# Optimization experiments

Hardware: AMD Instinct MI355X
Metric: run time of the kernel (lower is better)

Reference implementation:

```python
import jax, jax.numpy as jnp
import numpy as np

B, NS, NQ = 128, 128, 512
D_IN, D_OUT = 256, 64


def setup_inputs() -> dict:
    key = jax.random.key(0)
    ks = jax.random.split(key, 6)
    return {
        "phi_support": jax.random.normal(ks[0], (B, NS, D_IN), dtype=jnp.float32),
        "y_support": jax.random.normal(ks[1], (B, NS, D_OUT), dtype=jnp.float32),
        "phi_query": jax.random.normal(ks[2], (B, NQ, D_IN), dtype=jnp.float32),
        "y_query": jax.random.normal(ks[3], (B, NQ, D_OUT), dtype=jnp.float32),
        # xavier-uniform-ish params
        "m_prior": jax.random.uniform(ks[4], (D_IN, D_OUT), minval=-1.0, maxval=1.0) * np.sqrt(6.0 / (D_IN + D_OUT)),
        "S_inv_prior_asym": jax.random.uniform(ks[5], (D_IN, D_IN), minval=-1.0, maxval=1.0) * np.sqrt(6.0 / (2 * D_IN)),
        "sig_eps": jnp.array([0.1], dtype=jnp.float32),
    }


def reference(phi_support, y_support, phi_query, y_query, m_prior, S_inv_prior_asym, sig_eps):
    alpha = 1.0
    d_out = m_prior.shape[1]
    # prior precision (symmetric PSD by construction) and natural-param prior mean
    S_inv_prior = alpha * (S_inv_prior_asym @ S_inv_prior_asym.T)          # [D_in, D_in]
    m_prior_nat = S_inv_prior @ m_prior                                     # [D_in, D_out]
    # posterior precision / covariance per task (nobs > 0 branch)
    S_inv = jnp.einsum('bni,bnj->bij', phi_support, phi_support) + S_inv_prior  # [B, D_in, D_in]
    S = jnp.linalg.inv(S_inv)                                               # batched small inverse
    rhs = jnp.einsum('bni,bnk->bik', phi_support, y_support) + m_prior_nat  # [B, D_in, D_out]
    m = S @ rhs                                                             # [B, D_in, D_out]
    # predictive mean and spread
    mu = phi_query @ m                                                      # [B, Q, D_out]
    spread_fac = 1.0 + jnp.einsum('bqi,bij,bqj->bq', phi_query, S, phi_query)  # [B, Q]
    # sig = spread_fac (x) (eye * sig_eps) : diagonal [B, Q, D_out, D_out]
    diag = jnp.eye(d_out, dtype=mu.dtype) * sig_eps                         # [D_out, D_out]
    sig = spread_fac[..., None, None] * diag
    # nll: logdet of diagonal sig + quadratic form with its inverse (diag -> reciprocal)
    logdet = d_out * (jnp.log(spread_fac) + jnp.log(sig_eps))               # [B, Q]
    resid = y_query - mu
    quadf = jnp.sum(resid * resid, axis=-1) / (spread_fac * sig_eps)        # [B, Q]
    nll = logdet.mean() + quadf.mean()
    return mu, sig, nll
```

## Files before the change

### kernel.cpp

```cpp
#include <hip/hip_runtime.h>
#include <math.h>

#define B_T   128
#define NS    128
#define NQ    512
#define DIN   256
#define DOUT  64

#define MU_SIZE  (B_T*NQ*DOUT)
#define SIG_SIZE (B_T*NQ*DOUT*DOUT)
#define NLL_IDX  (MU_SIZE + SIG_SIZE)

__global__ __launch_bounds__(256) void k_prior_sp(const float* __restrict__ A,
                                                  double* __restrict__ Sp,
                                                  double* __restrict__ NLLACC) {
    __shared__ float Ai[16][260];
    __shared__ float Aj[16][260];
    int bi = blockIdx.x;
    int i0 = (bi >> 4) << 4;
    int j0 = (bi & 15) << 4;
    int tid = threadIdx.x;
    if (bi == 0 && tid == 0) NLLACC[0] = 0.0;
    for (int idx = tid; idx < 16 * 256; idx += 256) {
        int r = idx >> 8, c = idx & 255;
        Ai[r][c] = A[(i0 + r) * 256 + c];
        Aj[r][c] = A[(j0 + r) * 256 + c];
    }
    __syncthreads();
    int r = tid >> 4, c = tid & 15;
    double acc = 0.0;
    for (int k = 0; k < 256; ++k)
        acc += (double)Ai[r][k] * (double)Aj[c][k];
    Sp[(i0 + r) * 256 + (j0 + c)] = acc;
}

__global__ __launch_bounds__(64) void k_prior_mpn(const double* __restrict__ Sp,
                                                  const float* __restrict__ MP,
                                                  double* __restrict__ MPN) {
    int i = blockIdx.x, k = threadIdx.x;
    double acc = 0.0;
    for (int t = 0; t < 256; ++t)
        acc += Sp[i * 256 + t] * (double)MP[t * 64 + k];
    MPN[i * 64 + k] = acc;
}

__global__ __launch_bounds__(256) void k_build_G(const float* __restrict__ PHI,
                                                 const double* __restrict__ Sp,
                                                 double* __restrict__ G) {
    __shared__ float As[128][64];
    __shared__ float Bs[128][64];
    int b = blockIdx.x;
    int by = blockIdx.y;
    int ti = 0;
    while (((ti + 1) * (ti + 2)) / 2 <= by) ti++;
    int tj = by - (ti * (ti + 1)) / 2;
    int i0 = ti * 64, j0 = tj * 64;
    int tid = threadIdx.x;
    const float* Pb = PHI + b * (NS * DIN);
    for (int idx = tid; idx < 128 * 64; idx += 256) {
        int n = idx >> 6, c = idx & 63;
        As[n][c] = Pb[n * 256 + i0 + c];
        Bs[n][c] = Pb[n * 256 + j0 + c];
    }
    __syncthreads();
    int tx = tid & 15, ty = tid >> 4;
    double acc[4][4];
#pragma unroll
    for (int r = 0; r < 4; ++r)
#pragma unroll
        for (int s = 0; s < 4; ++s) acc[r][s] = 0.0;
    for (int n = 0; n < 128; ++n) {
        float a0 = As[n][4 * ty + 0], a1 = As[n][4 * ty + 1];
        float a2 = As[n][4 * ty + 2], a3 = As[n][4 * ty + 3];
        float b0 = Bs[n][4 * tx + 0], b1 = Bs[n][4 * tx + 1];
        float b2 = Bs[n][4 * tx + 2], b3 = Bs[n][4 * tx + 3];
        acc[0][0] += (double)a0 * b0; acc[0][1] += (double)a0 * b1;
        acc[0][2] += (double)a0 * b2; acc[0][3] += (double)a0 * b3;
        acc[1][0] += (double)a1 * b0; acc[1][1] += (double)a1 * b1;
        acc[1][2] += (double)a1 * b2; acc[1][3] += (double)a1 * b3;
        acc[2][0] += (double)a2 * b0; acc[2][1] += (double)a2 * b1;
        acc[2][2] += (double)a2 * b2; acc[2][3] += (double)a2 * b3;
        acc[3][0] += (double)a3 * b0; acc[3][1] += (double)a3 * b1;
        acc[3][2] += (double)a3 * b2; acc[3][3] += (double)a3 * b3;
    }
    double* Gb = G + b * 65536;
#pragma unroll
    for (int r = 0; r < 4; ++r) {
        int i = i0 + 4 * ty + r;
#pragma unroll
        for (int s = 0; s < 4; ++s) {
            int j = j0 + 4 * tx + s;
            Gb[i * 256 + j] = acc[r][s] + Sp[i * 256 + j];
        }
    }
}

__global__ __launch_bounds__(256) void k_build_rhs(const float* __restrict__ PHI,
                                                   const float* __restrict__ Y,
                                                   const double* __restrict__ MPN,
                                                   double* __restrict__ RHS) {
    __shared__ float As[128][64];
    __shared__ float Ys[128][64];
    int b = blockIdx.x, i0 = blockIdx.y * 64, tid = threadIdx.x;
    const float* Pb = PHI + b * (NS * DIN);
    const float* Yb = Y + b * (NS * DOUT);
    for (int idx = tid; idx < 128 * 64; idx += 256) {
        int n = idx >> 6, c = idx & 63;
        As[n][c] = Pb[n * 256 + i0 + c];
        Ys[n][c] = Yb[n * 64 + c];
    }
    __syncthreads();
    int tx = tid & 15, ty = tid >> 4;
    double acc[4][4];
#pragma unroll
    for (int r = 0; r < 4; ++r)
#pragma unroll
        for (int s = 0; s < 4; ++s) acc[r][s] = 0.0;
    for (int n = 0; n < 128; ++n) {
        float a0 = As[n][4 * ty + 0], a1 = As[n][4 * ty + 1];
        float a2 = As[n][4 * ty + 2], a3 = As[n][4 * ty + 3];
        float y0 = Ys[n][4 * tx + 0], y1 = Ys[n][4 * tx + 1];
        float y2 = Ys[n][4 * tx + 2], y3 = Ys[n][4 * tx + 3];
        acc[0][0] += (double)a0 * y0; acc[0][1] += (double)a0 * y1;
        acc[0][2] += (double)a0 * y2; acc[0][3] += (double)a0 * y3;
        acc[1][0] += (double)a1 * y0; acc[1][1] += (double)a1 * y1;
        acc[1][2] += (double)a1 * y2; acc[1][3] += (double)a1 * y3;
        acc[2][0] += (double)a2 * y0; acc[2][1] += (double)a2 * y1;
        acc[2][2] += (double)a2 * y2; acc[2][3] += (double)a2 * y3;
        acc[3][0] += (double)a3 * y0; acc[3][1] += (double)a3 * y1;
        acc[3][2] += (double)a3 * y2; acc[3][3] += (double)a3 * y3;
    }
    double* Rb = RHS + b * 16384;
#pragma unroll
    for (int r = 0; r < 4; ++r) {
        int i = i0 + 4 * ty + r;
#pragma unroll
        for (int s = 0; s < 4; ++s) {
            int kc = 4 * tx + s;
            Rb[i * 64 + kc] = acc[r][s] + MPN[i * 64 + kc];
        }
    }
}

__global__ __launch_bounds__(256) void k_cholinv(double* __restrict__ G,
                                                 double* __restrict__ LT,
                                                 double* __restrict__ TI,
                                                 float* __restrict__ TIF) {
    __shared__ double S[8192];
    int b = blockIdx.x, tid = threadIdx.x;
    double* Gb = G + b * 65536;
    double* LTb = LT + b * 65536;
    double* TIb = TI + b * 65536;
    float* TIFb = TIF + b * 65536;

    double* P = S;
#define PCH(p, r) P[(p) * 258 + (r)]
    for (int k0 = 0; k0 < 256; k0 += 16) {
        int rows = 256 - k0;
        for (int idx = tid; idx < rows * 16; idx += 256) {
            int r = k0 + (idx >> 4), p = idx & 15;
            PCH(p, r) = Gb[r * 256 + k0 + p];
        }
        __syncthreads();
        for (int p = 0; p < 16; ++p) {
            int k = k0 + p;
            if (tid >= k) {
                double v = PCH(p, tid);
                for (int p2 = 0; p2 < p; ++p2) v -= PCH(p2, tid) * PCH(p2, k);
                PCH(p, tid) = v;
            }
            __syncthreads();
            double d = sqrt(fmax(PCH(p, k), 1e-300));
            double inv = 1.0 / d;
            if (tid > k) PCH(p, tid) *= inv;
            else if (tid == k) PCH(p, tid) = d;
            __syncthreads();
        }
        for (int p = 0; p < 16; ++p) {
            int k = k0 + p;
            if (tid >= k) LTb[k * 256 + tid] = PCH(p, tid);
        }
        int ty = tid >> 4, tx = tid & 15;
        for (int i2 = k0 + 16 + 2 * ty; i2 < 256; i2 += 32) {
            double pa[16], pb[16];
#pragma unroll
            for (int p = 0; p < 16; ++p) { pa[p] = PCH(p, i2); pb[p] = PCH(p, i2 + 1); }
            for (int j2 = k0 + 16 + 2 * tx; j2 <= i2 + 1; j2 += 32) {
                double g00 = 0.0, g01 = 0.0, g10 = 0.0, g11 = 0.0;
#pragma unroll
                for (int p = 0; p < 16; ++p) {
                    double q0 = PCH(p, j2), q1 = PCH(p, j2 + 1);
                    g00 += pa[p] * q0; g01 += pa[p] * q1;
                    g10 += pb[p] * q0; g11 += pb[p] * q1;
                }
                if (j2 <= i2)     Gb[i2 * 256 + j2]           -= g00;
                if (j2 + 1 <= i2) Gb[i2 * 256 + j2 + 1]       -= g01;
                Gb[(i2 + 1) * 256 + j2] -= g10;
                if (j2 <= i2)     Gb[(i2 + 1) * 256 + j2 + 1] -= g11;
            }
        }
        __syncthreads();
    }
#undef PCH

    double* SHD = S;
    for (int idx = tid; idx < 65536; idx += 256) {
        int i = idx >> 8, k = idx & 255;
        if (k > i) { TIb[idx] = 0.0; TIFb[idx] = 0.0f; }
    }
    for (int idx = tid; idx < 8192; idx += 256) {
        int g = idx >> 10, rem = idx & 1023, k = rem >> 5, i = rem & 31;
        SHD[idx] = LTb[(32 * g + k) * 256 + 32 * g + i];
    }
    __syncthreads();
    {
        int g = tid >> 5, j = tid & 31;
        const double* D = SHD + g * 1024;
        double x[32];
#pragma unroll
        for (int i = 0; i < 32; ++i) {
            double s = (i == j) ? 1.0 : 0.0;
#pragma unroll
            for (int k = 0; k < i; ++k) {
                double lv = D[k * 32 + i];
                s -= (k >= j) ? lv * x[k] : 0.0;
            }
            double inv = 1.0 / D[i * 32 + i];
            x[i] = (i >= j) ? s * inv : 0.0;
        }
#pragma unroll
        for (int i = 0; i < 32; ++i) {
            int gi = 32 * g + i, gj = 32 * g + j;
            TIb[gi * 256 + gj] = x[i];
            TIFb[gi * 256 + gj] = (float)x[i];
        }
    }
    __syncthreads();
    double* Bsh = SHD;
    int j = tid & 31, ig = tid >> 5;
    for (int I = 1; I < 8; ++I) {
        for (int J = I - 1; J >= 0; --J) {
            double acc[4] = {0.0, 0.0, 0.0, 0.0};
            for (int K = J; K < I; ++K) {
                for (int kk = 0; kk < 32; ++kk) {
                    double tv = TIb[(32 * K + kk) * 256 + 32 * J + j];
#pragma unroll
                    for (int r = 0; r < 4; ++r) {
                        double lv = LTb[(32 * K + kk) * 256 + 32 * I + ig * 4 + r];
                        acc[r] += lv * tv;
                    }
                }
            }
            __syncthreads();
#pragma unroll
            for (int r = 0; r < 4; ++r) Bsh[(ig * 4 + r) * 32 + j] = acc[r];
            __syncthreads();
            double c[4] = {0.0, 0.0, 0.0, 0.0};
            for (int k = 0; k < 32; ++k) {
                double bv = Bsh[k * 32 + j];
#pragma unroll
                for (int r = 0; r < 4; ++r) {
                    double dv = TIb[(32 * I + ig * 4 + r) * 256 + 32 * I + k];
                    c[r] -= dv * bv;
                }
            }
#pragma unroll
            for (int r = 0; r < 4; ++r) {
                int gi = 32 * I + ig * 4 + r, gj = 32 * J + j;
                TIb[gi * 256 + gj] = c[r];
                TIFb[gi * 256 + gj] = (float)c[r];
            }
        }
        __syncthreads();
    }
}

__global__ __launch_bounds__(256) void k_gemm_Z(const double* __restrict__ TI,
                                                const double* __restrict__ RHS,
                                                double* __restrict__ Z) {
    __shared__ double As[32][64];
    __shared__ double Bs[64][64];
    int b = blockIdx.x, i0 = blockIdx.y * 32;
    int tid = threadIdx.x, c = tid & 63, rg = tid >> 6;
    const double* TIb = TI + b * 65536;
    const double* Rb = RHS + b * 16384;
    double* Zb = Z + b * 16384;
    double acc[8] = {};
    for (int k0 = 0; k0 <= i0; k0 += 64) {
        for (int idx = tid; idx < 2048; idx += 256) {
            int r = idx >> 6, kk = idx & 63;
            As[r][kk] = TIb[(i0 + r) * 256 + k0 + kk];
        }
        for (int idx = tid; idx < 4096; idx += 256) {
            int kk = idx >> 6, cc = idx & 63;
            Bs[kk][cc] = Rb[(k0 + kk) * 64 + cc];
        }
        __syncthreads();
        for (int kk = 0; kk < 64; ++kk) {
            double bv = Bs[kk][c];
#pragma unroll
            for (int r = 0; r < 8; ++r)
                acc[r] += As[rg * 8 + r][kk] * bv;
        }
        __syncthreads();
    }
#pragma unroll
    for (int r = 0; r < 8; ++r)
        Zb[(i0 + rg * 8 + r) * 64 + c] = acc[r];
}

__global__ __launch_bounds__(256) void k_gemm_M(const double* __restrict__ TI,
                                                const double* __restrict__ Z,
                                                double* __restrict__ M) {
    __shared__ double As[64][32];
    __shared__ double Bs[64][64];
    int b = blockIdx.x, i0 = blockIdx.y * 32;
    int tid = threadIdx.x, c = tid & 63, rg = tid >> 6;
    const double* TIb = TI + b * 65536;
    const double* Zb = Z + b * 16384;
    double* Mb = M + b * 16384;
    double acc[8] = {};
    for (int k0 = (i0 >> 6) << 6; k0 < 256; k0 += 64) {
        for (int idx = tid; idx < 2048; idx += 256) {
            int kk = idx >> 5, ri = idx & 31;
            As[kk][ri] = TIb[(k0 + kk) * 256 + i0 + ri];
        }
        for (int idx = tid; idx < 4096; idx += 256) {
            int kk = idx >> 6, cc = idx & 63;
            Bs[kk][cc] = Zb[(k0 + kk) * 64 + cc];
        }
        __syncthreads();
        for (int kk = 0; kk < 64; ++kk) {
            double bv = Bs[kk][c];
#pragma unroll
            for (int r = 0; r < 8; ++r)
                acc[r] += As[kk][rg * 8 + r] * bv;
        }
        __syncthreads();
    }
#pragma unroll
    for (int r = 0; r < 8; ++r)
        Mb[(i0 + rg * 8 + r) * 64 + c] = acc[r];
}

__global__ __launch_bounds__(256) void k_spread_gemm(const float* __restrict__ PHIQ,
                                                     const float* __restrict__ TIF,
                                                     float* __restrict__ PSUM) {
    __shared__ float Qs[64][65];
    __shared__ float Ts[64][65];
    int b = blockIdx.x, q0 = blockIdx.y * 64, I = blockIdx.z, i0 = I * 64;
    int tid = threadIdx.x, tx = tid & 15, ty = tid >> 4;
    const float* Qb = PHIQ + b * (NQ * DIN) + q0 * DIN;
    const float* Tb = TIF + b * 65536;
    float acc[4][4];
#pragma unroll
    for (int r = 0; r < 4; ++r)
#pragma unroll
        for (int s = 0; s < 4; ++s) acc[r][s] = 0.0f;
    for (int k0 = 0; k0 <= i0; k0 += 64) {
        for (int idx = tid; idx < 4096; idx += 256) {
            int r = idx >> 6, c = idx & 63;
            Qs[r][c] = Qb[r * 256 + k0 + c];
            Ts[c][r] = Tb[(i0 + r) * 256 + k0 + c];
        }
        __syncthreads();
        for (int kk = 0; kk < 64; ++kk) {
            float a0 = Qs[4 * ty + 0][kk], a1 = Qs[4 * ty + 1][kk];
            float a2 = Qs[4 * ty + 2][kk], a3 = Qs[4 * ty + 3][kk];
            float b0 = Ts[kk][4 * tx + 0], b1 = Ts[kk][4 * tx + 1];
            float b2 = Ts[kk][4 * tx + 2], b3 = Ts[kk][4 * tx + 3];
            acc[0][0] += a0 * b0; acc[0][1] += a0 * b1; acc[0][2] += a0 * b2; acc[0][3] += a0 * b3;
            acc[1][0] += a1 * b0; acc[1][1] += a1 * b1; acc[1][2] += a1 * b2; acc[1][3] += a1 * b3;
            acc[2][0] += a2 * b0; acc[2][1] += a2 * b1; acc[2][2] += a2 * b2; acc[2][3] += a2 * b3;
            acc[3][0] += a3 * b0; acc[3][1] += a3 * b1; acc[3][2] += a3 * b2; acc[3][3] += a3 * b3;
        }
        __syncthreads();
    }
#pragma unroll
    for (int r = 0; r < 4; ++r) {
        float p = acc[r][0] * acc[r][0] + acc[r][1] * acc[r][1]
                + acc[r][2] * acc[r][2] + acc[r][3] * acc[r][3];
        p += __shfl_down(p, 8, 16);
        p += __shfl_down(p, 4, 16);
        p += __shfl_down(p, 2, 16);
        p += __shfl_down(p, 1, 16);
        if (tx == 0) PSUM[(size_t)(b * 4 + I) * 512 + q0 + 4 * ty + r] = p;
    }
}

__global__ __launch_bounds__(256) void k_mu_nll(const float* __restrict__ PHIQ,
                                                const double* __restrict__ M,
                                                const float* __restrict__ YQ,
                                                const float* __restrict__ PSUM,
                                                const float* __restrict__ SE,
                                                float* __restrict__ SPREAD,
                                                double* __restrict__ NLLACC,
                                                float* __restrict__ MU) {
    __shared__ float Qs[64][65];
    __shared__ float Ms[64][64];
    __shared__ double nred[64];
    int b = blockIdx.x, q0 = blockIdx.y * 64, tid = threadIdx.x;
    int tx = tid & 15, ty = tid >> 4;
    const float* Qb = PHIQ + b * (NQ * DIN) + q0 * DIN;
    const double* Mb = M + b * 16384;
    float acc[4][4];
#pragma unroll
    for (int r = 0; r < 4; ++r)
#pragma unroll
        for (int s = 0; s < 4; ++s) acc[r][s] = 0.0f;
    for (int c0 = 0; c0 < 256; c0 += 64) {
        for (int idx = tid; idx < 4096; idx += 256) {
            int r = idx >> 6, c = idx & 63;
            Qs[r][c] = Qb[r * 256 + c0 + c];
            Ms[r][c] = (float)Mb[(c0 + r) * 64 + c];
        }
        __syncthreads();
        for (int kk = 0; kk < 64; ++kk) {
            float a0 = Qs[4 * ty + 0][kk], a1 = Qs[4 * ty + 1][kk];
            float a2 = Qs[4 * ty + 2][kk], a3 = Qs[4 * ty + 3][kk];
            float b0 = Ms[kk][4 * tx + 0], b1 = Ms[kk][4 * tx + 1];
            float b2 = Ms[kk][4 * tx + 2], b3 = Ms[kk][4 * tx + 3];
            acc[0][0] += a0 * b0; acc[0][1] += a0 * b1; acc[0][2] += a0 * b2; acc[0][3] += a0 * b3;
            acc[1][0] += a1 * b0; acc[1][1] += a1 * b1; acc[1][2] += a1 * b2; acc[1][3] += a1 * b3;
            acc[2][0] += a2 * b0; acc[2][1] += a2 * b1; acc[2][2] += a2 * b2; acc[2][3] += a2 * b3;
            acc[3][0] += a3 * b0; acc[3][1] += a3 * b1; acc[3][2] += a3 * b2; acc[3][3] += a3 * b3;
        }
        __syncthreads();
    }
    float se = SE[0];
#pragma unroll
    for (int r = 0; r < 4; ++r) {
        int q = q0 + 4 * ty + r;
        float4 v = make_float4(acc[r][0], acc[r][1], acc[r][2], acc[r][3]);
        *(float4*)&MU[(b * NQ + q) * 64 + 4 * tx] = v;
        float4 y = *(const float4*)&YQ[(size_t)(b * NQ + q) * 64 + 4 * tx];
        float dx = y.x - v.x, dy = y.y - v.y, dz = y.z - v.z, dw = y.w - v.w;
        float qs = dx * dx + dy * dy + dz * dz + dw * dw;
        qs += __shfl_down(qs, 8, 16);
        qs += __shfl_down(qs, 4, 16);
        qs += __shfl_down(qs, 2, 16);
        qs += __shfl_down(qs, 1, 16);
        if (tx == 0) {
            float sp = 1.0f + PSUM[(size_t)(b * 4 + 0) * 512 + q]
                            + PSUM[(size_t)(b * 4 + 1) * 512 + q]
                            + PSUM[(size_t)(b * 4 + 2) * 512 + q]
                            + PSUM[(size_t)(b * 4 + 3) * 512 + q];
            SPREAD[b * 512 + q] = sp;
            float val = 64.0f * (logf(sp) + logf(se)) + qs / (sp * se);
            nred[ty * 4 + r] = (double)val;
        }
    }
    __syncthreads();
    for (int s = 32; s > 0; s >>= 1) {
        if (tid < s) nred[tid] += nred[tid + s];
        __syncthreads();
    }
    if (tid == 0) atomicAdd(NLLACC, nred[0] * (1.0 / 65536.0));
}

__global__ void k_nll_final(const double* __restrict__ NLLACC,
                            float* __restrict__ out) {
    if (threadIdx.x == 0) out[NLL_IDX] = (float)NLLACC[0];
}

__global__ __launch_bounds__(256) void k_sig(const float* __restrict__ SPREAD,
                                             const float* __restrict__ SE,
                                             float* __restrict__ out) {
    __shared__ float sv_s;
    int bq = blockIdx.x, tid = threadIdx.x;
    if (tid == 0) sv_s = SPREAD[bq] * SE[0];
    __syncthreads();
    float sv = sv_s;
    float* base = out + (size_t)MU_SIZE + (size_t)bq * 4096;
    int i = tid >> 2;
    int jb = (tid & 3) << 4;
    int d = i - jb;
    float vals[16];
#pragma unroll
    for (int t = 0; t < 16; ++t) vals[t] = (t == d) ? sv : 0.0f;
    float4* p = (float4*)(base + tid * 16);
    p[0] = make_float4(vals[0], vals[1], vals[2], vals[3]);
    p[1] = make_float4(vals[4], vals[5], vals[6], vals[7]);
    p[2] = make_float4(vals[8], vals[9], vals[10], vals[11]);
    p[3] = make_float4(vals[12], vals[13], vals[14], vals[15]);
}

extern "C" void kernel_launch(void* const* d_in, const int* in_sizes, int n_in,
                              void* d_out, int out_size, void* d_ws, size_t ws_size,
                              hipStream_t stream) {
    const float* PHI_S = (const float*)d_in[0];
    const float* Y_S   = (const float*)d_in[1];
    const float* PHI_Q = (const float*)d_in[2];
    const float* Y_Q   = (const float*)d_in[3];
    const float* MP    = (const float*)d_in[4];
    const float* AP    = (const float*)d_in[5];
    const float* SE    = (const float*)d_in[6];
    float* out = (float*)d_out;

    double* scratch = (double*)(out + MU_SIZE);
    double* G    = scratch;
    double* LT   = G + 8388608;
    double* RHS  = LT + 8388608;
    double* Z    = RHS + 2097152;
    double* TI   = Z + 2097152;
    double* Spd  = TI + 8388608;
    double* MPN  = Spd + 65536;
    float*  TIF  = (float*)(MPN + 16384);
    float*  PSUM = TIF + 8388608;
    float*  SPREAD = (float*)d_ws;
    double* NLLACC = (double*)((char*)d_ws + 65536 * 4);

    k_prior_sp   <<<256, 256, 0, stream>>>(AP, Spd, NLLACC);
    k_prior_mpn  <<<256, 64, 0, stream>>>(Spd, MP, MPN);
    k_build_G    <<<dim3(B_T, 10), 256, 0, stream>>>(PHI_S, Spd, G);
    k_build_rhs  <<<dim3(B_T, 4), 256, 0, stream>>>(PHI_S, Y_S, MPN, RHS);
    k_cholinv    <<<B_T, 256, 0, stream>>>(G, LT, TI, TIF);
    k_gemm_Z     <<<dim3(B_T, 8), 256, 0, stream>>>(TI, RHS, Z);
    k_gemm_M     <<<dim3(B_T, 8), 256, 0, stream>>>(TI, Z, RHS);
    k_spread_gemm<<<dim3(B_T, 8, 4), 256, 0, stream>>>(PHI_Q, TIF, PSUM);
    k_mu_nll     <<<dim3(B_T, 8), 256, 0, stream>>>(PHI_Q, RHS, Y_Q, PSUM, SE,
                                                    SPREAD, NLLACC, out);
    k_nll_final  <<<1, 64, 0, stream>>>(NLLACC, out);
    k_sig        <<<65536, 256, 0, stream>>>(SPREAD, SE, out);
}
```

Measured before the change: 2.244 ms.

## Widen Cholesky panel to 32 columns and fold small prior kernels into neighbors

The blocked Cholesky panel width grows from 16 to 32, which halves the number of panel iterations and global trailing-update passes over G, at the cost of more per-thread registers (32-element pa/pb arrays) and more serial per-column work in the panel. The prior mean-natural-param GEMM moves into extra blocks of k_build_rhs, and its addition is deferred to k_gemm_Z's load. The nll final write moves into k_sig, which removes two tiny launches. Index arithmetic in mu output also switches to size_t.

```diff
diff --git a/kernel.cpp b/kernel.cpp
--- a/kernel.cpp
+++ b/kernel.cpp
@@ -32,16 +32,6 @@
     for (int k = 0; k < 256; ++k)
         acc += (double)Ai[r][k] * (double)Aj[c][k];
     Sp[(i0 + r) * 256 + (j0 + c)] = acc;
-}
-
-__global__ __launch_bounds__(64) void k_prior_mpn(const double* __restrict__ Sp,
-                                                  const float* __restrict__ MP,
-                                                  double* __restrict__ MPN) {
-    int i = blockIdx.x, k = threadIdx.x;
-    double acc = 0.0;
-    for (int t = 0; t < 256; ++t)
-        acc += Sp[i * 256 + t] * (double)MP[t * 64 + k];
-    MPN[i * 64 + k] = acc;
 }
 
 __global__ __launch_bounds__(256) void k_build_G(const float* __restrict__ PHI,
@@ -97,11 +87,25 @@
 
 __global__ __launch_bounds__(256) void k_build_rhs(const float* __restrict__ PHI,
                                                    const float* __restrict__ Y,
-                                                   const double* __restrict__ MPN,
-                                                   double* __restrict__ RHS) {
+                                                   const float* __restrict__ MP,
+                                                   const double* __restrict__ Sp,
+                                                   double* __restrict__ RHS,
+                                                   double* __restrict__ MPNo) {
+    int b = blockIdx.x, by = blockIdx.y, tid = threadIdx.x;
+    if (by == 4) {
+        if (b >= 4) return;
+        for (int out = tid; out < 4096; out += 256) {
+            int r = 64 * b + (out >> 6), cc = out & 63;
+            double acc = 0.0;
+            for (int t = 0; t < 256; ++t)
+                acc += Sp[r * 256 + t] * (double)MP[t * 64 + cc];
+            MPNo[r * 64 + cc] = acc;
+        }
+        return;
+    }
     __shared__ float As[128][64];
     __shared__ float Ys[128][64];
-    int b = blockIdx.x, i0 = blockIdx.y * 64, tid = threadIdx.x;
+    int i0 = by * 64;
     const float* Pb = PHI + b * (NS * DIN);
     const float* Yb = Y + b * (NS * DOUT);
     for (int idx = tid; idx < 128 * 64; idx += 256) {
@@ -135,10 +139,8 @@
     for (int r = 0; r < 4; ++r) {
         int i = i0 + 4 * ty + r;
 #pragma unroll
-        for (int s = 0; s < 4; ++s) {
-            int kc = 4 * tx + s;
-            Rb[i * 64 + kc] = acc[r][s] + MPN[i * 64 + kc];
-        }
+        for (int s = 0; s < 4; ++s)
+            Rb[i * 64 + 4 * tx + s] = acc[r][s];
     }
 }
 
@@ -146,7 +148,7 @@
                                                  double* __restrict__ LT,
                                                  double* __restrict__ TI,
                                                  float* __restrict__ TIF) {
-    __shared__ double S[8192];
+    __shared__ double S[8256];
     int b = blockIdx.x, tid = threadIdx.x;
     double* Gb = G + b * 65536;
     double* LTb = LT + b * 65536;
@@ -155,14 +157,14 @@
 
     double* P = S;
 #define PCH(p, r) P[(p) * 258 + (r)]
-    for (int k0 = 0; k0 < 256; k0 += 16) {
+    for (int k0 = 0; k0 < 256; k0 += 32) {
         int rows = 256 - k0;
-        for (int idx = tid; idx < rows * 16; idx += 256) {
-            int r = k0 + (idx >> 4), p = idx & 15;
+        for (int idx = tid; idx < rows * 32; idx += 256) {
+            int r = k0 + (idx >> 5), p = idx & 31;
             PCH(p, r) = Gb[r * 256 + k0 + p];
         }
         __syncthreads();
-        for (int p = 0; p < 16; ++p) {
+        for (int p = 0; p < 32; ++p) {
             int k = k0 + p;
             if (tid >= k) {
                 double v = PCH(p, tid);
@@ -176,19 +178,19 @@
             else if (tid == k) PCH(p, tid) = d;
             __syncthreads();
         }
-        for (int p = 0; p < 16; ++p) {
+        for (int p = 0; p < 32; ++p) {
             int k = k0 + p;
             if (tid >= k) LTb[k * 256 + tid] = PCH(p, tid);
         }
         int ty = tid >> 4, tx = tid & 15;
-        for (int i2 = k0 + 16 + 2 * ty; i2 < 256; i2 += 32) {
-            double pa[16], pb[16];
-#pragma unroll
-            for (int p = 0; p < 16; ++p) { pa[p] = PCH(p, i2); pb[p] = PCH(p, i2 + 1); }
-            for (int j2 = k0 + 16 + 2 * tx; j2 <= i2 + 1; j2 += 32) {
+        for (int i2 = k0 + 32 + 2 * ty; i2 < 256; i2 += 32) {
+            double pa[32], pb[32];
+#pragma unroll
+            for (int p = 0; p < 32; ++p) { pa[p] = PCH(p, i2); pb[p] = PCH(p, i2 + 1); }
+            for (int j2 = k0 + 32 + 2 * tx; j2 <= i2 + 1; j2 += 32) {
                 double g00 = 0.0, g01 = 0.0, g10 = 0.0, g11 = 0.0;
 #pragma unroll
-                for (int p = 0; p < 16; ++p) {
+                for (int p = 0; p < 32; ++p) {
                     double q0 = PCH(p, j2), q1 = PCH(p, j2 + 1);
                     g00 += pa[p] * q0; g01 += pa[p] * q1;
                     g10 += pb[p] * q0; g11 += pb[p] * q1;
@@ -277,6 +279,7 @@
 
 __global__ __launch_bounds__(256) void k_gemm_Z(const double* __restrict__ TI,
                                                 const double* __restrict__ RHS,
+                                                const double* __restrict__ MPN,
                                                 double* __restrict__ Z) {
     __shared__ double As[32][64];
     __shared__ double Bs[64][64];
@@ -293,7 +296,7 @@
         }
         for (int idx = tid; idx < 4096; idx += 256) {
             int kk = idx >> 6, cc = idx & 63;
-            Bs[kk][cc] = Rb[(k0 + kk) * 64 + cc];
+            Bs[kk][cc] = Rb[(k0 + kk) * 64 + cc] + MPN[(k0 + kk) * 64 + cc];
         }
         __syncthreads();
         for (int kk = 0; kk < 64; ++kk) {
@@ -432,8 +435,8 @@
     for (int r = 0; r < 4; ++r) {
         int q = q0 + 4 * ty + r;
         float4 v = make_float4(acc[r][0], acc[r][1], acc[r][2], acc[r][3]);
-        *(float4*)&MU[(b * NQ + q) * 64 + 4 * tx] = v;
-        float4 y = *(const float4*)&YQ[(size_t)(b * NQ + q) * 64 + 4 * tx];
+        *(float4*)&MU[((size_t)b * NQ + q) * 64 + 4 * tx] = v;
+        float4 y = *(const float4*)&YQ[((size_t)b * NQ + q) * 64 + 4 * tx];
         float dx = y.x - v.x, dy = y.y - v.y, dz = y.z - v.z, dw = y.w - v.w;
         float qs = dx * dx + dy * dy + dz * dz + dw * dw;
         qs += __shfl_down(qs, 8, 16);
@@ -458,16 +461,13 @@
     if (tid == 0) atomicAdd(NLLACC, nred[0] * (1.0 / 65536.0));
 }
 
-__global__ void k_nll_final(const double* __restrict__ NLLACC,
-                            float* __restrict__ out) {
-    if (threadIdx.x == 0) out[NLL_IDX] = (float)NLLACC[0];
-}
-
 __global__ __launch_bounds__(256) void k_sig(const float* __restrict__ SPREAD,
                                              const float* __restrict__ SE,
+                                             const double* __restrict__ NLLACC,
                                              float* __restrict__ out) {
     __shared__ float sv_s;
     int bq = blockIdx.x, tid = threadIdx.x;
+    if (bq == 0 && tid == 0) out[NLL_IDX] = (float)NLLACC[0];
     if (tid == 0) sv_s = SPREAD[bq] * SE[0];
     __syncthreads();
     float sv = sv_s;
@@ -511,15 +511,13 @@
     double* NLLACC = (double*)((char*)d_ws + 65536 * 4);
 
     k_prior_sp   <<<256, 256, 0, stream>>>(AP, Spd, NLLACC);
-    k_prior_mpn  <<<256, 64, 0, stream>>>(Spd, MP, MPN);
     k_build_G    <<<dim3(B_T, 10), 256, 0, stream>>>(PHI_S, Spd, G);
-    k_build_rhs  <<<dim3(B_T, 4), 256, 0, stream>>>(PHI_S, Y_S, MPN, RHS);
+    k_build_rhs  <<<dim3(B_T, 5), 256, 0, stream>>>(PHI_S, Y_S, MP, Spd, RHS, MPN);
     k_cholinv    <<<B_T, 256, 0, stream>>>(G, LT, TI, TIF);
-    k_gemm_Z     <<<dim3(B_T, 8), 256, 0, stream>>>(TI, RHS, Z);
+    k_gemm_Z     <<<dim3(B_T, 8), 256, 0, stream>>>(TI, RHS, MPN, Z);
     k_gemm_M     <<<dim3(B_T, 8), 256, 0, stream>>>(TI, Z, RHS);
     k_spread_gemm<<<dim3(B_T, 8, 4), 256, 0, stream>>>(PHI_Q, TIF, PSUM);
     k_mu_nll     <<<dim3(B_T, 8), 256, 0, stream>>>(PHI_Q, RHS, Y_Q, PSUM, SE,
                                                     SPREAD, NLLACC, out);
-    k_nll_final  <<<1, 64, 0, stream>>>(NLLACC, out);
-    k_sig        <<<65536, 256, 0, stream>>>(SPREAD, SE, out);
-}
+    k_sig        <<<65536, 256, 0, stream>>>(SPREAD, SE, NLLACC, out);
+}
```

After: 2.433 ms. 1.08x slower.
